# Optimization experiments

Measured on AMD Instinct MI355X. Metric: run time of the kernel, lower is better.

## Reference

```python
import jax, jax.numpy as jnp
import numpy as np

B = 4096
D_IN = 1024
D_H = 1024


def setup_inputs() -> dict:
    key = jax.random.key(0)
    ks = jax.random.split(key, 11)
    s = 1.0 / np.sqrt(D_IN + D_H)  # torch nn.Linear default init scale
    def w(k):
        return jax.random.uniform(k, (D_H, D_IN + D_H), jnp.float32, -s, s)
    def b(k):
        return jax.random.uniform(k, (D_H,), jnp.float32, -s, s)
    return {
        "inputs": jax.random.normal(ks[0], (B, D_IN), jnp.float32),
        "h_prev": jax.random.normal(ks[1], (B, D_H), jnp.float32),
        "c_prev": jax.random.normal(ks[2], (B, D_H), jnp.float32),
        "W_i": w(ks[3]), "b_i": b(ks[4]),
        "W_f": w(ks[5]), "b_f": b(ks[6]),
        "W_c": w(ks[7]), "b_c": b(ks[8]),
        "W_o": w(ks[9]), "b_o": b(ks[10]),
    }


def reference(inputs, h_prev, c_prev, W_i, b_i, W_f, b_f, W_c, b_c, W_o, b_o):
    combined = jnp.concatenate([inputs, h_prev], axis=1)  # [B, D_IN+D_H]
    # Fuse the four gate projections into one GEMM: [B, 4*D_H]
    W = jnp.concatenate([W_i, W_f, W_c, W_o], axis=0)      # [4*D_H, D_IN+D_H]
    bvec = jnp.concatenate([b_i, b_f, b_c, b_o], axis=0)   # [4*D_H]
    z = combined @ W.T + bvec
    zi, zf, zc, zo = jnp.split(z, 4, axis=1)
    i_gate = jax.nn.sigmoid(zi)
    f_gate = jax.nn.sigmoid(zf)
    c_gate = jnp.tanh(zc)
    o_gate = jax.nn.sigmoid(zo)
    c_next = f_gate * c_prev + i_gate * c_gate
    h_next = o_gate * jnp.tanh(c_next)
    return (h_next, c_next)
```

## Files before the change

### kernel.cpp

```cpp
#include <hip/hip_runtime.h>
#include <stdint.h>

#define B_SZ 4096
#define D_K  2048
#define DH   1024

#define BM   128
#define BN_H 32
#define BKI  128
#define NIT  (D_K / BKI)

typedef __attribute__((ext_vector_type(4))) int intx4;

__device__ __forceinline__ float fast_sigmoid(float x) {
  return 1.0f / (1.0f + __expf(-x));
}
__device__ __forceinline__ float fast_tanh(float x) {
  return 2.0f / (1.0f + __expf(-2.0f * x)) - 1.0f;
}

#define SQRT2048 45.254833995939045f

__global__ __launch_bounds__(256) void prep_i8(
    const float* __restrict__ xin, const float* __restrict__ hprev,
    const float* __restrict__ Wi, const float* __restrict__ Wf,
    const float* __restrict__ Wc, const float* __restrict__ Wo,
    int8_t* __restrict__ Ai8, int8_t* __restrict__ Wq8,
    float* __restrict__ sA)
{
  __shared__ float wm[4];
  const int r = blockIdx.x;
  const int t = threadIdx.x;
  const int k = t * 8;
  float v[8];

  if (r < B_SZ) {
    const int m = r;
    const float* src = (k < 1024) ? (xin + (size_t)m * 1024 + k)
                                  : (hprev + (size_t)m * 1024 + (k - 1024));
    float4 f0 = *(const float4*)src;
    float4 f1 = *(const float4*)(src + 4);
    v[0]=f0.x; v[1]=f0.y; v[2]=f0.z; v[3]=f0.w;
    v[4]=f1.x; v[5]=f1.y; v[6]=f1.z; v[7]=f1.w;
    float lm = 0.f;
    #pragma unroll
    for (int j = 0; j < 8; ++j) lm = fmaxf(lm, fabsf(v[j]));
    #pragma unroll
    for (int mask = 32; mask >= 1; mask >>= 1)
      lm = fmaxf(lm, __shfl_xor(lm, mask, 64));
    const int wave = t >> 6, lane = t & 63;
    if (lane == 0) wm[wave] = lm;
    __syncthreads();
    float rowmax = fmaxf(fmaxf(wm[0], wm[1]), fmaxf(wm[2], wm[3]));
    rowmax = fmaxf(rowmax, 1e-20f);
    if (t == 0) sA[m] = rowmax * (1.0f / 127.0f);
    const float qs = 127.0f / rowmax;
    uint32_t lo = 0, hi = 0;
    #pragma unroll
    for (int j = 0; j < 4; ++j) {
      int q = __float2int_rn(v[j] * qs);
      lo |= (uint32_t)(q & 255) << (8 * j);
    }
    #pragma unroll
    for (int j = 0; j < 4; ++j) {
      int q = __float2int_rn(v[4 + j] * qs);
      hi |= (uint32_t)(q & 255) << (8 * j);
    }
    uint2 out; out.x = lo; out.y = hi;
    *(uint2*)(Ai8 + (size_t)m * D_K + k) = out;
  } else {
    const int n = r - B_SZ;
    const int g = n >> 10, h = n & 1023;
    const float* wsrc = (g == 0) ? Wi : (g == 1) ? Wf : (g == 2) ? Wc : Wo;
    const float* src = wsrc + (size_t)h * D_K + k;
    float4 f0 = *(const float4*)src;
    float4 f1 = *(const float4*)(src + 4);
    v[0]=f0.x; v[1]=f0.y; v[2]=f0.z; v[3]=f0.w;
    v[4]=f1.x; v[5]=f1.y; v[6]=f1.z; v[7]=f1.w;
    const float qs = 127.0f * SQRT2048;
    uint32_t lo = 0, hi = 0;
    #pragma unroll
    for (int j = 0; j < 4; ++j) {
      int q = min(127, max(-127, __float2int_rn(v[j] * qs)));
      lo |= (uint32_t)(q & 255) << (8 * j);
    }
    #pragma unroll
    for (int j = 0; j < 4; ++j) {
      int q = min(127, max(-127, __float2int_rn(v[4 + j] * qs)));
      hi |= (uint32_t)(q & 255) << (8 * j);
    }
    uint2 out; out.x = lo; out.y = hi;
    *(uint2*)(Wq8 + (size_t)n * D_K + k) = out;
  }
}

__global__ __launch_bounds__(256, 2) void lstm_gemm_i8(
    const int8_t* __restrict__ A,
    const int8_t* __restrict__ W,
    const float* __restrict__ sA,
    const float* __restrict__ bi, const float* __restrict__ bfv,
    const float* __restrict__ bc, const float* __restrict__ bo,
    const float* __restrict__ cprev,
    float* __restrict__ out)
{
  __shared__ __align__(16) int8_t lA[2][BM * BKI];
  __shared__ __align__(16) int8_t lB[2][128 * BKI];

  const int m0 = blockIdx.x * BM;
  const int h0 = blockIdx.y * BN_H;
  const int tid = threadIdx.x;
  const int wave = tid >> 6;
  const int lane = tid & 63;
  const int wm = wave >> 1;
  const int wn = wave & 1;

  const int sr8 = lane >> 3;
  const int sch = lane & 7;
  const int gc  = sch ^ sr8;

  const int8_t* aSrc[4];
  const int8_t* bSrc[4];
  int dOff[4];
  #pragma unroll
  for (int j = 0; j < 4; ++j) {
    int r = wave * 32 + j * 8 + sr8;
    aSrc[j] = A + (size_t)(m0 + r) * D_K + gc * 16;
    bSrc[j] = W + (size_t)(wave * DH + h0 + j * 8 + sr8) * D_K + gc * 16;
    dOff[j] = r * BKI + sch * 16;
  }

  intx4 acc[4][4];
  #pragma unroll
  for (int i = 0; i < 4; ++i)
    #pragma unroll
    for (int j = 0; j < 4; ++j)
      acc[i][j] = (intx4){0, 0, 0, 0};

  const int fr = lane & 15;
  const int q  = lane >> 4;
  const int cx0 = ((q + 0) ^ (fr & 7)) * 16;
  const int cx1 = ((q + 4) ^ (fr & 7)) * 16;

#define STAGE(buf, kt) do {                                                  \
    const int _ko = (kt) * BKI;                                              \
    _Pragma("unroll")                                                        \
    for (int j = 0; j < 4; ++j)                                              \
      __builtin_amdgcn_global_load_lds(                                      \
          (const __attribute__((address_space(1))) void*)(aSrc[j] + _ko),    \
          (__attribute__((address_space(3))) void*)&lA[buf][dOff[j]], 16, 0, 0); \
    _Pragma("unroll")                                                        \
    for (int j = 0; j < 4; ++j)                                              \
      __builtin_amdgcn_global_load_lds(                                      \
          (const __attribute__((address_space(1))) void*)(bSrc[j] + _ko),    \
          (__attribute__((address_space(3))) void*)&lB[buf][dOff[j]], 16, 0, 0); \
  } while (0)

#define COMPUTE(buf) do {                                                    \
    _Pragma("unroll")                                                        \
    for (int kk = 0; kk < 2; ++kk) {                                         \
      const int cx = kk ? cx1 : cx0;                                         \
      intx4 bq[4];                                                           \
      _Pragma("unroll")                                                      \
      for (int g = 0; g < 4; ++g)                                            \
        bq[g] = *(const intx4*)&lB[buf][(g * 32 + wn * 16 + fr) * BKI + cx]; \
      _Pragma("unroll")                                                      \
      for (int i = 0; i < 4; ++i) {                                          \
        intx4 aq = *(const intx4*)&lA[buf][(wm * 64 + i * 16 + fr) * BKI + cx]; \
        acc[i][0] = __builtin_amdgcn_mfma_i32_16x16x64_i8(aq, bq[0], acc[i][0], 0, 0, 0); \
        acc[i][1] = __builtin_amdgcn_mfma_i32_16x16x64_i8(aq, bq[1], acc[i][1], 0, 0, 0); \
        acc[i][2] = __builtin_amdgcn_mfma_i32_16x16x64_i8(aq, bq[2], acc[i][2], 0, 0, 0); \
        acc[i][3] = __builtin_amdgcn_mfma_i32_16x16x64_i8(aq, bq[3], acc[i][3], 0, 0, 0); \
      }                                                                      \
    }                                                                        \
  } while (0)

  STAGE(0, 0);
  __syncthreads();

  #pragma unroll 1
  for (int kt = 0; kt < NIT; kt += 2) {
    if (kt + 1 < NIT) STAGE(1, kt + 1);
    COMPUTE(0);
    __syncthreads();
    if (kt + 2 < NIT) STAGE(0, kt + 2);
    COMPUTE(1);
    __syncthreads();
  }

#undef STAGE
#undef COMPUTE

  const int col = lane & 15;
  const int rq = lane >> 4;
  const int h = h0 + wn * 16 + col;
  const float sWc = (1.0f / SQRT2048) * (1.0f / 127.0f);
  const float bias_i = bi[h], bias_f = bfv[h], bias_c = bc[h], bias_o = bo[h];
  float* hout = out;
  float* cout = out + (size_t)B_SZ * DH;
  #pragma unroll
  for (int i = 0; i < 4; ++i) {
    int mb = m0 + wm * 64 + i * 16 + rq * 4;
    #pragma unroll
    for (int r = 0; r < 4; ++r) {
      int m = mb + r;
      float fz = sA[m] * sWc;
      float zi = (float)acc[i][0][r] * fz + bias_i;
      float zf = (float)acc[i][1][r] * fz + bias_f;
      float zc = (float)acc[i][2][r] * fz + bias_c;
      float zo = (float)acc[i][3][r] * fz + bias_o;
      float ig = fast_sigmoid(zi);
      float fg = fast_sigmoid(zf);
      float cg = fast_tanh(zc);
      float og = fast_sigmoid(zo);
      float cp = cprev[(size_t)m * DH + h];
      float cn = fg * cp + ig * cg;
      float hn = og * fast_tanh(cn);
      hout[(size_t)m * DH + h] = hn;
      cout[(size_t)m * DH + h] = cn;
    }
  }
}

extern "C" void kernel_launch(void* const* d_in, const int* in_sizes, int n_in,
                              void* d_out, int out_size, void* d_ws, size_t ws_size,
                              hipStream_t stream)
{
  const float* xin   = (const float*)d_in[0];
  const float* hprev = (const float*)d_in[1];
  const float* cprev = (const float*)d_in[2];
  const float* Wi    = (const float*)d_in[3];
  const float* bi    = (const float*)d_in[4];
  const float* Wf    = (const float*)d_in[5];
  const float* bfv   = (const float*)d_in[6];
  const float* Wc    = (const float*)d_in[7];
  const float* bc    = (const float*)d_in[8];
  const float* Wo    = (const float*)d_in[9];
  const float* bo    = (const float*)d_in[10];
  float* out = (float*)d_out;

  int8_t* Ai8 = (int8_t*)d_ws;
  int8_t* Wq8 = Ai8 + (size_t)B_SZ * D_K;
  float*  sA  = (float*)(Wq8 + (size_t)4 * DH * D_K);

  prep_i8<<<2 * B_SZ, 256, 0, stream>>>(
      xin, hprev, Wi, Wf, Wc, Wo, Ai8, Wq8, sA);

  dim3 grid(B_SZ / BM, DH / BN_H);
  lstm_gemm_i8<<<grid, 256, 0, stream>>>(
      Ai8, Wq8, sA, bi, bfv, bc, bo, cprev, out);
}
```

Baseline: 181.7 us.

## Use 512-thread 256-row tiles with split B loads and finer vmcnt waits

Doubles the M tile to 256 rows with 8 waves per block, so each wave loads only half as many B rows and the shared weight tile is reused across more rows. Full __syncthreads are replaced by explicit s_waitcnt vmcnt counts plus raw barriers, letting the prefetch of the next stage stay in flight while the current stage is computed. MFMA sections are wrapped in s_setprio to favour math waves. LDS use rises and the grid halves, so fewer blocks can be resident, and the hand-counted vmcnt values must exactly match the number of outstanding loads.

```diff
diff --git a/kernel.cpp b/kernel.cpp
--- a/kernel.cpp
+++ b/kernel.cpp
@@ -5,7 +5,7 @@
 #define D_K  2048
 #define DH   1024
 
-#define BM   128
+#define BM   256
 #define BN_H 32
 #define BKI  128
 #define NIT  (D_K / BKI)
@@ -94,7 +94,7 @@
   }
 }
 
-__global__ __launch_bounds__(256, 2) void lstm_gemm_i8(
+__global__ __launch_bounds__(512, 1) void lstm_gemm_i8(
     const int8_t* __restrict__ A,
     const int8_t* __restrict__ W,
     const float* __restrict__ sA,
@@ -119,14 +119,20 @@
   const int gc  = sch ^ sr8;
 
   const int8_t* aSrc[4];
-  const int8_t* bSrc[4];
-  int dOff[4];
+  int dOffA[4];
   #pragma unroll
   for (int j = 0; j < 4; ++j) {
     int r = wave * 32 + j * 8 + sr8;
     aSrc[j] = A + (size_t)(m0 + r) * D_K + gc * 16;
-    bSrc[j] = W + (size_t)(wave * DH + h0 + j * 8 + sr8) * D_K + gc * 16;
-    dOff[j] = r * BKI + sch * 16;
+    dOffA[j] = r * BKI + sch * 16;
+  }
+  const int8_t* bSrc[2];
+  int dOffB[2];
+  #pragma unroll
+  for (int j = 0; j < 2; ++j) {
+    int r = wave * 16 + j * 8 + sr8;
+    bSrc[j] = W + (size_t)((r >> 5) * DH + h0 + (r & 31)) * D_K + gc * 16;
+    dOffB[j] = r * BKI + sch * 16;
   }
 
   intx4 acc[4][4];
@@ -147,12 +153,12 @@
     for (int j = 0; j < 4; ++j)                                              \
       __builtin_amdgcn_global_load_lds(                                      \
           (const __attribute__((address_space(1))) void*)(aSrc[j] + _ko),    \
-          (__attribute__((address_space(3))) void*)&lA[buf][dOff[j]], 16, 0, 0); \
+          (__attribute__((address_space(3))) void*)&lA[buf][dOffA[j]], 16, 0, 0); \
     _Pragma("unroll")                                                        \
-    for (int j = 0; j < 4; ++j)                                              \
+    for (int j = 0; j < 2; ++j)                                              \
       __builtin_amdgcn_global_load_lds(                                      \
           (const __attribute__((address_space(1))) void*)(bSrc[j] + _ko),    \
-          (__attribute__((address_space(3))) void*)&lB[buf][dOff[j]], 16, 0, 0); \
+          (__attribute__((address_space(3))) void*)&lB[buf][dOffB[j]], 16, 0, 0); \
   } while (0)
 
 #define COMPUTE(buf) do {                                                    \
@@ -163,6 +169,7 @@
       _Pragma("unroll")                                                      \
       for (int g = 0; g < 4; ++g)                                            \
         bq[g] = *(const intx4*)&lB[buf][(g * 32 + wn * 16 + fr) * BKI + cx]; \
+      __builtin_amdgcn_s_setprio(1);                                         \
       _Pragma("unroll")                                                      \
       for (int i = 0; i < 4; ++i) {                                          \
         intx4 aq = *(const intx4*)&lA[buf][(wm * 64 + i * 16 + fr) * BKI + cx]; \
@@ -171,20 +178,28 @@
         acc[i][2] = __builtin_amdgcn_mfma_i32_16x16x64_i8(aq, bq[2], acc[i][2], 0, 0, 0); \
         acc[i][3] = __builtin_amdgcn_mfma_i32_16x16x64_i8(aq, bq[3], acc[i][3], 0, 0, 0); \
       }                                                                      \
+      __builtin_amdgcn_s_setprio(0);                                         \
     }                                                                        \
   } while (0)
 
   STAGE(0, 0);
-  __syncthreads();
 
   #pragma unroll 1
   for (int kt = 0; kt < NIT; kt += 2) {
-    if (kt + 1 < NIT) STAGE(1, kt + 1);
+    STAGE(1, kt + 1);
+    asm volatile("s_waitcnt vmcnt(6)" ::: "memory");
+    __builtin_amdgcn_s_barrier();
     COMPUTE(0);
-    __syncthreads();
-    if (kt + 2 < NIT) STAGE(0, kt + 2);
+    __builtin_amdgcn_s_barrier();
+    if (kt + 2 < NIT) {
+      STAGE(0, kt + 2);
+      asm volatile("s_waitcnt vmcnt(6)" ::: "memory");
+    } else {
+      asm volatile("s_waitcnt vmcnt(0)" ::: "memory");
+    }
+    __builtin_amdgcn_s_barrier();
     COMPUTE(1);
-    __syncthreads();
+    __builtin_amdgcn_s_barrier();
   }
 
 #undef STAGE
@@ -246,6 +261,6 @@
       xin, hprev, Wi, Wf, Wc, Wo, Ai8, Wq8, sA);
 
   dim3 grid(B_SZ / BM, DH / BN_H);
-  lstm_gemm_i8<<<grid, 256, 0, stream>>>(
+  lstm_gemm_i8<<<grid, 512, 0, stream>>>(
       Ai8, Wq8, sA, bi, bfv, bc, bo, cprev, out);
 }
```

Result: slower. 185.7 us (+2.2%).

## Enlarge GEMM tile to 256x256 with 8 waves and phased barrier-interleaved pipeline

Applied to the files above, without the earlier changes.

Doubles the block tile to 256 rows by 64 hidden units (256 weight rows across the four gates) with 512 threads per block, so each loaded operand is reused more. The main loop is reworked into four sub-phases per K step: each issues its LDS fragment reads and splits the next tile's A and B global-to-LDS loads across phases, then separates them from the MFMA bursts with explicit barriers and s_setprio. The aim is to cut global and LDS traffic per MFMA and overlap loads with compute. In exchange it uses 128 KB of LDS and allows only one block per CU, and the grid shrinks to 256 blocks, which risks under-filling the device and exposing latency.

```diff
diff --git a/kernel.cpp b/kernel.cpp
--- a/kernel.cpp
+++ b/kernel.cpp
@@ -5,8 +5,8 @@
 #define D_K  2048
 #define DH   1024
 
-#define BM   128
-#define BN_H 32
+#define BM   256
+#define BN_H 64
 #define BKI  128
 #define NIT  (D_K / BKI)
 
@@ -94,7 +94,7 @@
   }
 }
 
-__global__ __launch_bounds__(256, 2) void lstm_gemm_i8(
+__global__ __launch_bounds__(512, 1) void lstm_gemm_i8(
     const int8_t* __restrict__ A,
     const int8_t* __restrict__ W,
     const float* __restrict__ sA,
@@ -104,15 +104,15 @@
     float* __restrict__ out)
 {
   __shared__ __align__(16) int8_t lA[2][BM * BKI];
-  __shared__ __align__(16) int8_t lB[2][128 * BKI];
+  __shared__ __align__(16) int8_t lB[2][256 * BKI];
 
   const int m0 = blockIdx.x * BM;
   const int h0 = blockIdx.y * BN_H;
   const int tid = threadIdx.x;
   const int wave = tid >> 6;
   const int lane = tid & 63;
-  const int wm = wave >> 1;
-  const int wn = wave & 1;
+  const int wm = wave >> 2;
+  const int wn = wave & 3;
 
   const int sr8 = lane >> 3;
   const int sch = lane & 7;
@@ -125,13 +125,13 @@
   for (int j = 0; j < 4; ++j) {
     int r = wave * 32 + j * 8 + sr8;
     aSrc[j] = A + (size_t)(m0 + r) * D_K + gc * 16;
-    bSrc[j] = W + (size_t)(wave * DH + h0 + j * 8 + sr8) * D_K + gc * 16;
+    bSrc[j] = W + (size_t)((r >> 6) * DH + h0 + (r & 63)) * D_K + gc * 16;
     dOff[j] = r * BKI + sch * 16;
   }
 
-  intx4 acc[4][4];
+  intx4 acc[8][4];
   #pragma unroll
-  for (int i = 0; i < 4; ++i)
+  for (int i = 0; i < 8; ++i)
     #pragma unroll
     for (int j = 0; j < 4; ++j)
       acc[i][j] = (intx4){0, 0, 0, 0};
@@ -141,13 +141,17 @@
   const int cx0 = ((q + 0) ^ (fr & 7)) * 16;
   const int cx1 = ((q + 4) ^ (fr & 7)) * 16;
 
-#define STAGE(buf, kt) do {                                                  \
+#define STAGE_A(buf, kt) do {                                                \
     const int _ko = (kt) * BKI;                                              \
     _Pragma("unroll")                                                        \
     for (int j = 0; j < 4; ++j)                                              \
       __builtin_amdgcn_global_load_lds(                                      \
           (const __attribute__((address_space(1))) void*)(aSrc[j] + _ko),    \
           (__attribute__((address_space(3))) void*)&lA[buf][dOff[j]], 16, 0, 0); \
+  } while (0)
+
+#define STAGE_B(buf, kt) do {                                                \
+    const int _ko = (kt) * BKI;                                              \
     _Pragma("unroll")                                                        \
     for (int j = 0; j < 4; ++j)                                              \
       __builtin_amdgcn_global_load_lds(                                      \
@@ -155,40 +159,59 @@
           (__attribute__((address_space(3))) void*)&lB[buf][dOff[j]], 16, 0, 0); \
   } while (0)
 
-#define COMPUTE(buf) do {                                                    \
-    _Pragma("unroll")                                                        \
-    for (int kk = 0; kk < 2; ++kk) {                                         \
-      const int cx = kk ? cx1 : cx0;                                         \
-      intx4 bq[4];                                                           \
-      _Pragma("unroll")                                                      \
-      for (int g = 0; g < 4; ++g)                                            \
-        bq[g] = *(const intx4*)&lB[buf][(g * 32 + wn * 16 + fr) * BKI + cx]; \
-      _Pragma("unroll")                                                      \
-      for (int i = 0; i < 4; ++i) {                                          \
-        intx4 aq = *(const intx4*)&lA[buf][(wm * 64 + i * 16 + fr) * BKI + cx]; \
-        acc[i][0] = __builtin_amdgcn_mfma_i32_16x16x64_i8(aq, bq[0], acc[i][0], 0, 0, 0); \
-        acc[i][1] = __builtin_amdgcn_mfma_i32_16x16x64_i8(aq, bq[1], acc[i][1], 0, 0, 0); \
-        acc[i][2] = __builtin_amdgcn_mfma_i32_16x16x64_i8(aq, bq[2], acc[i][2], 0, 0, 0); \
-        acc[i][3] = __builtin_amdgcn_mfma_i32_16x16x64_i8(aq, bq[3], acc[i][3], 0, 0, 0); \
-      }                                                                      \
-    }                                                                        \
-  } while (0)
-
-  STAGE(0, 0);
-  __syncthreads();
+  STAGE_A(0, 0);
+  STAGE_B(0, 0);
+  asm volatile("s_waitcnt vmcnt(0)" ::: "memory");
+  __builtin_amdgcn_s_barrier();
 
   #pragma unroll 1
-  for (int kt = 0; kt < NIT; kt += 2) {
-    if (kt + 1 < NIT) STAGE(1, kt + 1);
-    COMPUTE(0);
-    __syncthreads();
-    if (kt + 2 < NIT) STAGE(0, kt + 2);
-    COMPUTE(1);
-    __syncthreads();
-  }
-
-#undef STAGE
-#undef COMPUTE
+  for (int t = 0; t < NIT; ++t) {
+    const int b = t & 1;
+    intx4 bq[4][2];
+
+    #pragma unroll
+    for (int p = 0; p < 4; ++p) {
+      if (p == 0) {
+        #pragma unroll
+        for (int g = 0; g < 4; ++g) {
+          const int rb = (g * 64 + wn * 16 + fr) * BKI;
+          bq[g][0] = *(const intx4*)&lB[b][rb + cx0];
+          bq[g][1] = *(const intx4*)&lB[b][rb + cx1];
+        }
+      }
+      intx4 aq[2][2];
+      #pragma unroll
+      for (int s = 0; s < 2; ++s) {
+        const int ra = (wm * 128 + (2 * p + s) * 16 + fr) * BKI;
+        aq[s][0] = *(const intx4*)&lA[b][ra + cx0];
+        aq[s][1] = *(const intx4*)&lA[b][ra + cx1];
+      }
+      if (p == 0 && t + 1 < NIT) STAGE_A(b ^ 1, t + 1);
+      if (p == 1 && t + 1 < NIT) STAGE_B(b ^ 1, t + 1);
+
+      asm volatile("" ::: "memory");
+      __builtin_amdgcn_s_barrier();
+      asm volatile("s_waitcnt lgkmcnt(0)" ::: "memory");
+
+      __builtin_amdgcn_s_setprio(1);
+      #pragma unroll
+      for (int kk = 0; kk < 2; ++kk)
+        #pragma unroll
+        for (int s = 0; s < 2; ++s)
+          #pragma unroll
+          for (int g = 0; g < 4; ++g)
+            acc[2 * p + s][g] = __builtin_amdgcn_mfma_i32_16x16x64_i8(
+                aq[s][kk], bq[g][kk], acc[2 * p + s][g], 0, 0, 0);
+      __builtin_amdgcn_s_setprio(0);
+
+      if (p == 3) asm volatile("s_waitcnt vmcnt(0)" ::: "memory");
+      asm volatile("" ::: "memory");
+      __builtin_amdgcn_s_barrier();
+    }
+  }
+
+#undef STAGE_A
+#undef STAGE_B
 
   const int col = lane & 15;
   const int rq = lane >> 4;
@@ -198,16 +221,16 @@
   float* hout = out;
   float* cout = out + (size_t)B_SZ * DH;
   #pragma unroll
-  for (int i = 0; i < 4; ++i) {
-    int mb = m0 + wm * 64 + i * 16 + rq * 4;
+  for (int mf = 0; mf < 8; ++mf) {
+    int mb = m0 + wm * 128 + mf * 16 + rq * 4;
     #pragma unroll
     for (int r = 0; r < 4; ++r) {
       int m = mb + r;
       float fz = sA[m] * sWc;
-      float zi = (float)acc[i][0][r] * fz + bias_i;
-      float zf = (float)acc[i][1][r] * fz + bias_f;
-      float zc = (float)acc[i][2][r] * fz + bias_c;
-      float zo = (float)acc[i][3][r] * fz + bias_o;
+      float zi = (float)acc[mf][0][r] * fz + bias_i;
+      float zf = (float)acc[mf][1][r] * fz + bias_f;
+      float zc = (float)acc[mf][2][r] * fz + bias_c;
+      float zo = (float)acc[mf][3][r] * fz + bias_o;
       float ig = fast_sigmoid(zi);
       float fg = fast_sigmoid(zf);
       float cg = fast_tanh(zc);
@@ -246,6 +269,6 @@
       xin, hprev, Wi, Wf, Wc, Wo, Ai8, Wq8, sA);
 
   dim3 grid(B_SZ / BM, DH / BN_H);
-  lstm_gemm_i8<<<grid, 256, 0, stream>>>(
+  lstm_gemm_i8<<<grid, 512, 0, stream>>>(
       Ai8, Wq8, sA, bi, bfv, bc, bo, cprev, out);
 }
```

Result: faster. 173.6 us (-4.5%).

## Restructure int8 GEMM main loop with split barriers, setprio and coalesced prep loads

Applied to the files above, without the earlier changes.

The GEMM main loop is rewritten as a single-step double-buffered loop. Each half-tile first loads its LDS fragments into registers, then hits a barrier, then issues its MFMA cluster under raised wave priority, and waits for outstanding global-to-LDS loads only at the end of the tile. The aim is to overlap LDS reads, MFMA issue and the async global loads more tightly than full __syncthreads would. The prep kernel also changes its thread-to-column mapping so each thread reads one float4 from the x half and one from the h half, giving coalesced 16-byte loads instead of strided 32-byte chunks. The cost is more barriers per tile and reliance on hand-placed waitcnt ordering for correctness.

```diff
diff --git a/kernel.cpp b/kernel.cpp
--- a/kernel.cpp
+++ b/kernel.cpp
@@ -31,15 +31,13 @@
   __shared__ float wm[4];
   const int r = blockIdx.x;
   const int t = threadIdx.x;
-  const int k = t * 8;
+  const int k4 = t * 4;
   float v[8];
 
   if (r < B_SZ) {
     const int m = r;
-    const float* src = (k < 1024) ? (xin + (size_t)m * 1024 + k)
-                                  : (hprev + (size_t)m * 1024 + (k - 1024));
-    float4 f0 = *(const float4*)src;
-    float4 f1 = *(const float4*)(src + 4);
+    float4 f0 = *(const float4*)(xin   + (size_t)m * 1024 + k4);
+    float4 f1 = *(const float4*)(hprev + (size_t)m * 1024 + k4);
     v[0]=f0.x; v[1]=f0.y; v[2]=f0.z; v[3]=f0.w;
     v[4]=f1.x; v[5]=f1.y; v[6]=f1.z; v[7]=f1.w;
     float lm = 0.f;
@@ -66,15 +64,15 @@
       int q = __float2int_rn(v[4 + j] * qs);
       hi |= (uint32_t)(q & 255) << (8 * j);
     }
-    uint2 out; out.x = lo; out.y = hi;
-    *(uint2*)(Ai8 + (size_t)m * D_K + k) = out;
+    *(uint32_t*)(Ai8 + (size_t)m * D_K + k4)        = lo;
+    *(uint32_t*)(Ai8 + (size_t)m * D_K + 1024 + k4) = hi;
   } else {
     const int n = r - B_SZ;
     const int g = n >> 10, h = n & 1023;
     const float* wsrc = (g == 0) ? Wi : (g == 1) ? Wf : (g == 2) ? Wc : Wo;
-    const float* src = wsrc + (size_t)h * D_K + k;
-    float4 f0 = *(const float4*)src;
-    float4 f1 = *(const float4*)(src + 4);
+    const float* src = wsrc + (size_t)h * D_K;
+    float4 f0 = *(const float4*)(src + k4);
+    float4 f1 = *(const float4*)(src + 1024 + k4);
     v[0]=f0.x; v[1]=f0.y; v[2]=f0.z; v[3]=f0.w;
     v[4]=f1.x; v[5]=f1.y; v[6]=f1.z; v[7]=f1.w;
     const float qs = 127.0f * SQRT2048;
@@ -89,8 +87,8 @@
       int q = min(127, max(-127, __float2int_rn(v[4 + j] * qs)));
       hi |= (uint32_t)(q & 255) << (8 * j);
     }
-    uint2 out; out.x = lo; out.y = hi;
-    *(uint2*)(Wq8 + (size_t)n * D_K + k) = out;
+    *(uint32_t*)(Wq8 + (size_t)n * D_K + k4)        = lo;
+    *(uint32_t*)(Wq8 + (size_t)n * D_K + 1024 + k4) = hi;
   }
 }
 
@@ -155,40 +153,46 @@
           (__attribute__((address_space(3))) void*)&lB[buf][dOff[j]], 16, 0, 0); \
   } while (0)
 
-#define COMPUTE(buf) do {                                                    \
-    _Pragma("unroll")                                                        \
-    for (int kk = 0; kk < 2; ++kk) {                                         \
-      const int cx = kk ? cx1 : cx0;                                         \
-      intx4 bq[4];                                                           \
-      _Pragma("unroll")                                                      \
-      for (int g = 0; g < 4; ++g)                                            \
-        bq[g] = *(const intx4*)&lB[buf][(g * 32 + wn * 16 + fr) * BKI + cx]; \
-      _Pragma("unroll")                                                      \
-      for (int i = 0; i < 4; ++i) {                                          \
-        intx4 aq = *(const intx4*)&lA[buf][(wm * 64 + i * 16 + fr) * BKI + cx]; \
-        acc[i][0] = __builtin_amdgcn_mfma_i32_16x16x64_i8(aq, bq[0], acc[i][0], 0, 0, 0); \
-        acc[i][1] = __builtin_amdgcn_mfma_i32_16x16x64_i8(aq, bq[1], acc[i][1], 0, 0, 0); \
-        acc[i][2] = __builtin_amdgcn_mfma_i32_16x16x64_i8(aq, bq[2], acc[i][2], 0, 0, 0); \
-        acc[i][3] = __builtin_amdgcn_mfma_i32_16x16x64_i8(aq, bq[3], acc[i][3], 0, 0, 0); \
-      }                                                                      \
-    }                                                                        \
-  } while (0)
-
   STAGE(0, 0);
-  __syncthreads();
+  asm volatile("s_waitcnt vmcnt(0)" ::: "memory");
+  __builtin_amdgcn_s_barrier();
 
   #pragma unroll 1
-  for (int kt = 0; kt < NIT; kt += 2) {
-    if (kt + 1 < NIT) STAGE(1, kt + 1);
-    COMPUTE(0);
-    __syncthreads();
-    if (kt + 2 < NIT) STAGE(0, kt + 2);
-    COMPUTE(1);
-    __syncthreads();
+  for (int t = 0; t < NIT; ++t) {
+    const int b = t & 1;
+    if (t + 1 < NIT) STAGE(b ^ 1, t + 1);
+
+    #pragma unroll
+    for (int kk = 0; kk < 2; ++kk) {
+      const int cx = kk ? cx1 : cx0;
+      intx4 bq[4], aq[4];
+      #pragma unroll
+      for (int g = 0; g < 4; ++g)
+        bq[g] = *(const intx4*)&lB[b][(g * 32 + wn * 16 + fr) * BKI + cx];
+      #pragma unroll
+      for (int i = 0; i < 4; ++i)
+        aq[i] = *(const intx4*)&lA[b][(wm * 64 + i * 16 + fr) * BKI + cx];
+
+      asm volatile("" ::: "memory");
+      __builtin_amdgcn_s_barrier();
+
+      __builtin_amdgcn_s_setprio(1);
+      #pragma unroll
+      for (int i = 0; i < 4; ++i) {
+        acc[i][0] = __builtin_amdgcn_mfma_i32_16x16x64_i8(aq[i], bq[0], acc[i][0], 0, 0, 0);
+        acc[i][1] = __builtin_amdgcn_mfma_i32_16x16x64_i8(aq[i], bq[1], acc[i][1], 0, 0, 0);
+        acc[i][2] = __builtin_amdgcn_mfma_i32_16x16x64_i8(aq[i], bq[2], acc[i][2], 0, 0, 0);
+        acc[i][3] = __builtin_amdgcn_mfma_i32_16x16x64_i8(aq[i], bq[3], acc[i][3], 0, 0, 0);
+      }
+      __builtin_amdgcn_s_setprio(0);
+
+      if (kk == 1) asm volatile("s_waitcnt vmcnt(0)" ::: "memory");
+      asm volatile("" ::: "memory");
+      __builtin_amdgcn_s_barrier();
+    }
   }
 
 #undef STAGE
-#undef COMPUTE
 
   const int col = lane & 15;
   const int rq = lane >> 4;
```

New measurement: 177.6 us. -2.3%, faster.
